# Kernel optimization log

Measured on AMD Instinct MI355X. Metric: run time of the kernel, lower is better.

The kernel has to match this reference:

```python
import jax, jax.numpy as jnp
import numpy as np

B, S, D, E = 4, 4096, 2048, 64
NOISE_STD = 1.0


def setup_inputs() -> dict:
    key = jax.random.key(0)
    k1, k2, k3, k4 = jax.random.split(key, 4)
    x = jax.random.normal(k1, (B, S, D), dtype=jnp.float32)
    lim = float(np.sqrt(6.0 / (D + E)))  # glorot_uniform
    W_gate = jax.random.uniform(k2, (D, E), jnp.float32, -lim, lim)
    # keras inits noise_dense kernel to zeros; use tiny random values so the
    # noise path is numerically exercised (zeros would make it trivially ln(2)).
    W_noise = 0.02 * jax.random.normal(k3, (D, E), dtype=jnp.float32)
    noise = jax.random.normal(k4, (B * S, E), dtype=jnp.float32)
    return {"x": x, "W_gate": W_gate, "W_noise": W_noise, "noise": noise, "top_k": 2}


def reference(x, W_gate, W_noise, noise, top_k):
    b, s, d = x.shape
    e = W_gate.shape[1]
    xf = x.reshape(-1, d)                         # [N, D], N = b*s
    gate_logits = xf @ W_gate                     # [N, E]
    # training-mode noise injection
    noise_logits = xf @ W_noise                   # [N, E]
    nstd = jax.nn.softplus(noise_logits) * (NOISE_STD / (e * e))
    gate_logits = gate_logits + noise * nstd
    # top-k mask + masked softmax
    top_vals, top_idx = jax.lax.top_k(gate_logits, top_k)   # [N, K]
    n = gate_logits.shape[0]
    mask = jnp.zeros_like(gate_logits).at[jnp.arange(n)[:, None], top_idx].set(1.0)
    masked_logits = jnp.where(mask > 0, gate_logits, jnp.float32(-1e9))
    expert_weights = jax.nn.softmax(masked_logits, axis=-1)  # [N, E]
    raw_gate_probs = jax.nn.softmax(gate_logits, axis=-1)    # [N, E]
    expert_weights = expert_weights.reshape(b, s, e)
    expert_indices = top_idx.reshape(b, s, top_k).astype(jnp.int32)
    return expert_weights, expert_indices, gate_logits, raw_gate_probs
```

## Files before the change

kernel.cpp:

```cpp
#include <hip/hip_runtime.h>
#include <math.h>


typedef _Float16 f16;
typedef f16  f16x4  __attribute__((ext_vector_type(4)));
typedef f16  f16x8  __attribute__((ext_vector_type(8)));
typedef float f32x16 __attribute__((ext_vector_type(16)));

constexpr int NROWS = 16384;
constexpr int DDIM  = 2048;
constexpr int NE    = 64;
constexpr int BM    = 32;
constexpr int KI    = 32;
constexpr int NITER = 1024 / KI;
constexpr float NSCALE = 1.0f / 4096.0f;

__device__ __forceinline__ int a_off(int buf, int h, int s, int v) {
    return (((buf * 2 + h) * 2 + s) * 2 + v) * 1024;
}

__device__ __forceinline__ float softplus_f(float x) {
    return fmaxf(x, 0.0f) + log1pf(expf(-fabsf(x)));
}

__device__ __forceinline__ void tile_bar() {
    asm volatile("s_waitcnt lgkmcnt(0)" ::: "memory");
    __builtin_amdgcn_sched_barrier(0);
    __builtin_amdgcn_s_barrier();
    __builtin_amdgcn_sched_barrier(0);
}

__global__ __launch_bounds__(256) void wprep_kernel(
    const float* __restrict__ Wg, const float* __restrict__ Wn,
    f16* __restrict__ ws)
{
    int t = blockIdx.x * 256 + threadIdx.x;
    int S = t >> 8;
    int f = (t >> 6) & 3;
    int l = t & 63;
    int k0  = S * 16 + (l >> 5) * 8;
    int col = f * 32 + (l & 31);
    const float* src = (col < NE) ? (Wg + col) : (Wn + col - NE);
    f16x8 hp, lp;
    #pragma unroll
    for (int j = 0; j < 8; ++j) {
        float w  = src[(size_t)(k0 + j) * NE];
        f16 h    = (f16)w;
        float hf = (float)h;
        hp[j] = h;
        lp[j] = (f16)((w - hf) * 64.0f);
    }
    size_t base = (size_t)(S * 4 + f) * 1024;
    *(f16x8*)(ws + base + l * 8)       = hp;
    *(f16x8*)(ws + base + 512 + l * 8) = lp;
}

__global__ __launch_bounds__(512, 4) void gemm_gating(
    const float* __restrict__ x, const f16* __restrict__ wfrag,
    const float* __restrict__ noise,
    float* __restrict__ out_w, float* __restrict__ out_idx,
    float* __restrict__ out_logits, float* __restrict__ out_probs)
{
    __shared__ __align__(16) char smem[49152];
    const int tid = threadIdx.x;
    const int l   = tid & 63;
    const int w   = tid >> 6;
    const int h   = w >> 2;
    const int f   = w & 3;
    const int row0 = blockIdx.x * BM;

    f32x16 acc1, acc2;
    #pragma unroll
    for (int r = 0; r < 16; ++r) { acc1[r] = 0.0f; acc2[r] = 0.0f; }

    const int h_s = w >> 2, s_s = (w >> 1) & 1, j4 = w & 1;
    const float* aSrc = x + (size_t)(row0 + (l & 31)) * DDIM
                          + h_s * 1024 + s_s * 16 + (l >> 5) * 8 + j4 * 4;
    auto loadA = [&](int t) -> float4 {
        return *(const float4*)(aSrc + (size_t)t * KI);
    };
    auto cvtWrite = [&](float4 xv, int tt) {
        int buf = tt & 3;
        float xs[4] = {xv.x, xv.y, xv.z, xv.w};
        f16x4 hi, lo;
        #pragma unroll
        for (int j = 0; j < 4; ++j) {
            f16 hh   = (f16)xs[j];
            float hf = (float)hh;
            hi[j] = hh;
            lo[j] = (f16)((xs[j] - hf) * 64.0f);
        }
        *(f16x4*)(smem + a_off(buf, h_s, s_s, 0) + l * 16 + j4 * 8) = hi;
        *(f16x4*)(smem + a_off(buf, h_s, s_s, 1) + l * 16 + j4 * 8) = lo;
    };

    const f16* bBase = wfrag + (size_t)f * 1024 + l * 8;
    f16x8 bh0c, bl0c, bh1c, bl1c, bh0n, bl0n, bh1n, bl1n;
    auto loadB = [&](int t, f16x8& H0, f16x8& L0, f16x8& H1, f16x8& L1) {
        const f16* p = bBase + (size_t)(h * 64 + t * 2) * 4096;
        H0 = *(const f16x8*)p;
        L0 = *(const f16x8*)(p + 512);
        H1 = *(const f16x8*)(p + 4096);
        L1 = *(const f16x8*)(p + 4096 + 512);
    };

    auto compute = [&](int t) {
        int buf = t & 3;
        #pragma unroll
        for (int s = 0; s < 2; ++s) {
            f16x8 Ah = *(const f16x8*)(smem + a_off(buf, h, s, 0) + l * 16);
            f16x8 Al = *(const f16x8*)(smem + a_off(buf, h, s, 1) + l * 16);
            f16x8 Bh = s ? bh1c : bh0c;
            f16x8 Bl = s ? bl1c : bl0c;
            acc1 = __builtin_amdgcn_mfma_f32_32x32x16_f16(Ah, Bh, acc1, 0, 0, 0);
            acc2 = __builtin_amdgcn_mfma_f32_32x32x16_f16(Ah, Bl, acc2, 0, 0, 0);
            acc2 = __builtin_amdgcn_mfma_f32_32x32x16_f16(Al, Bh, acc2, 0, 0, 0);
        }
    };

    float4 r0 = loadA(0);
    float4 r1 = loadA(1);
    loadB(0, bh0c, bl0c, bh1c, bl1c);
    float4 sc = loadA(2);
    float4 sm = loadA(3);
    cvtWrite(r0, 0);
    cvtWrite(r1, 1);

    for (int t = 0; t < NITER; ++t) {
        tile_bar();
        float4 sn = sc;
        if (t + 4 < NITER) sn = loadA(t + 4);
        if (t + 1 < NITER) loadB(t + 1, bh0n, bl0n, bh1n, bl1n);
        if (t + 2 < NITER) cvtWrite(sc, t + 2);
        compute(t);
        sc = sm; sm = sn;
        bh0c = bh0n; bl0c = bl0n; bh1c = bh1n; bl1c = bl1n;
    }
    __syncthreads();

    float* mg  = (float*)(smem + 32768);
    if (h == 1) {
        #pragma unroll
        for (int r = 0; r < 16; ++r) {
            float cv = fmaf(acc2[r], 0.015625f, acc1[r]);
            int row = (r & 3) + 8 * (r >> 2) + 4 * (l >> 5);
            int col = f * 32 + (l & 31);
            mg[row * 128 + col] = cv;
        }
    }
    __syncthreads();

    float* lgf = (float*)smem;
    if (h == 0) {
        #pragma unroll
        for (int r = 0; r < 16; ++r) {
            float cv = fmaf(acc2[r], 0.015625f, acc1[r]);
            int row = (r & 3) + 8 * (r >> 2) + 4 * (l >> 5);
            int col = f * 32 + (l & 31);
            lgf[row * 132 + col] = cv + mg[row * 128 + col];
        }
    }
    __syncthreads();

    {
        const int pr = tid & 31;
        const int c4 = tid >> 5;
        const int n1 = row0 + pr;
        float4 G  = *(const float4*)(lgf + pr * 132 + c4 * 4);
        float4 NL = *(const float4*)(lgf + pr * 132 + 64 + c4 * 4);
        float4 NZ = *(const float4*)(noise + (size_t)n1 * NE + c4 * 4);
        G.x += NZ.x * softplus_f(NL.x) * NSCALE;
        G.y += NZ.y * softplus_f(NL.y) * NSCALE;
        G.z += NZ.z * softplus_f(NL.z) * NSCALE;
        G.w += NZ.w * softplus_f(NL.w) * NSCALE;
        *(float4*)(lgf + pr * 132 + c4 * 4) = G;
        *(float4*)(out_logits + (size_t)n1 * NE + c4 * 4) = G;
    }
    __syncthreads();

    if (w < 4) {
        const int g2   = l >> 3;
        const int c    = l & 7;
        const int row2 = w * 8 + g2;
        const int n2   = row0 + row2;

        float mv[8];
        {
            const float4* mr = (const float4*)(lgf + row2 * 132 + c * 8);
            float4 m0 = mr[0], m1 = mr[1];
            mv[0]=m0.x; mv[1]=m0.y; mv[2]=m0.z; mv[3]=m0.w;
            mv[4]=m1.x; mv[5]=m1.y; mv[6]=m1.z; mv[7]=m1.w;
        }
        float v0 = -INFINITY, v1 = -INFINITY;
        int i0 = 0, i1 = 0;
        #pragma unroll
        for (int j = 0; j < 8; ++j) {
            float v = mv[j]; int e = c * 8 + j;
            if (v > v0) { v1 = v0; i1 = i0; v0 = v; i0 = e; }
            else if (v > v1) { v1 = v; i1 = e; }
        }
        #pragma unroll
        for (int m = 1; m <= 4; m <<= 1) {
            float ov0 = __shfl_xor(v0, m), ov1 = __shfl_xor(v1, m);
            int   oi0 = __shfl_xor(i0, m), oi1 = __shfl_xor(i1, m);
            if (ov0 > v0) {
                bool keep = (v0 > ov1);
                v1 = keep ? v0 : ov1; i1 = keep ? i0 : oi1;
                v0 = ov0; i0 = oi0;
            } else if (ov0 > v1) {
                v1 = ov0; i1 = oi0;
            }
        }
        const int srcl = l & 56;
        v0 = __shfl(v0, srcl); i0 = __shfl(i0, srcl);
        v1 = __shfl(v1, srcl); i1 = __shfl(i1, srcl);

        float se = 0.0f;
        #pragma unroll
        for (int j = 0; j < 8; ++j) se += expf(mv[j] - v0);
        se += __shfl_xor(se, 1); se += __shfl_xor(se, 2); se += __shfl_xor(se, 4);
        float inv_se = 1.0f / se;

        float t  = expf(v1 - v0);
        float w0 = 1.0f / (1.0f + t);
        float w1 = t * w0;

        float pr[8], wt[8];
        #pragma unroll
        for (int j = 0; j < 8; ++j) {
            int e = c * 8 + j;
            pr[j] = expf(mv[j] - v0) * inv_se;
            wt[j] = (e == i0) ? w0 : ((e == i1) ? w1 : 0.0f);
        }
        *(float4*)(out_probs + (size_t)n2 * NE + c * 8)     = make_float4(pr[0], pr[1], pr[2], pr[3]);
        *(float4*)(out_probs + (size_t)n2 * NE + c * 8 + 4) = make_float4(pr[4], pr[5], pr[6], pr[7]);
        *(float4*)(out_w + (size_t)n2 * NE + c * 8)         = make_float4(wt[0], wt[1], wt[2], wt[3]);
        *(float4*)(out_w + (size_t)n2 * NE + c * 8 + 4)     = make_float4(wt[4], wt[5], wt[6], wt[7]);
        if (c == 0) {
            *(float2*)(out_idx + (size_t)n2 * 2) = make_float2((float)i0, (float)i1);
        }
    }
}

extern "C" void kernel_launch(void* const* d_in, const int* in_sizes, int n_in,
                              void* d_out, int out_size, void* d_ws, size_t ws_size,
                              hipStream_t stream) {
    (void)in_sizes; (void)n_in; (void)ws_size; (void)out_size;
    const float* x     = (const float*)d_in[0];
    const float* Wg    = (const float*)d_in[1];
    const float* Wn    = (const float*)d_in[2];
    const float* noise = (const float*)d_in[3];
    float* out        = (float*)d_out;
    float* out_w      = out;
    float* out_idx    = out + (size_t)NROWS * NE;
    float* out_logits = out_idx + (size_t)NROWS * 2;
    float* out_probs  = out_logits + (size_t)NROWS * NE;
    f16* wfrag = (f16*)d_ws;

    wprep_kernel<<<128, 256, 0, stream>>>(Wg, Wn, wfrag);
    gemm_gating<<<NROWS / BM, 512, 0, stream>>>(
        x, wfrag, noise, out_w, out_idx, out_logits, out_probs);
}
```

Before: 56.08 us.

## Unroll K-loop by four with static smem buffers and double-buffered B fragments

Restructures the main GEMM loop into a 4-way manually unrolled body with compile-time shared-memory buffer indices and two ping-ponged sets of B-fragment registers. Compute on the current buffer is issued before the next global loads and conversion writes, and the custom lgkmcnt/sched_barrier tile barrier is replaced with plain __syncthreads. The aim is to remove the register rotation copies and dynamic buffer indexing, and to give the scheduler more freedom to overlap loads with MFMA. In exchange it uses more registers and gives up the explicit scheduling barriers, so instruction placement is left to the compiler.

New measurement: 52.52 us. -6.3%, faster.

```diff
diff --git a/kernel.cpp b/kernel.cpp
--- a/kernel.cpp
+++ b/kernel.cpp
@@ -12,7 +12,6 @@
 constexpr int NE    = 64;
 constexpr int BM    = 32;
 constexpr int KI    = 32;
-constexpr int NITER = 1024 / KI;
 constexpr float NSCALE = 1.0f / 4096.0f;
 
 __device__ __forceinline__ int a_off(int buf, int h, int s, int v) {
@@ -21,13 +20,6 @@
 
 __device__ __forceinline__ float softplus_f(float x) {
     return fmaxf(x, 0.0f) + log1pf(expf(-fabsf(x)));
-}
-
-__device__ __forceinline__ void tile_bar() {
-    asm volatile("s_waitcnt lgkmcnt(0)" ::: "memory");
-    __builtin_amdgcn_sched_barrier(0);
-    __builtin_amdgcn_s_barrier();
-    __builtin_amdgcn_sched_barrier(0);
 }
 
 __global__ __launch_bounds__(256) void wprep_kernel(
@@ -79,8 +71,7 @@
     auto loadA = [&](int t) -> float4 {
         return *(const float4*)(aSrc + (size_t)t * KI);
     };
-    auto cvtWrite = [&](float4 xv, int tt) {
-        int buf = tt & 3;
+    auto cvtWrite = [&](float4 xv, int buf) {
         float xs[4] = {xv.x, xv.y, xv.z, xv.w};
         f16x4 hi, lo;
         #pragma unroll
@@ -95,50 +86,65 @@
     };
 
     const f16* bBase = wfrag + (size_t)f * 1024 + l * 8;
-    f16x8 bh0c, bl0c, bh1c, bl1c, bh0n, bl0n, bh1n, bl1n;
-    auto loadB = [&](int t, f16x8& H0, f16x8& L0, f16x8& H1, f16x8& L1) {
-        const f16* p = bBase + (size_t)(h * 64 + t * 2) * 4096;
-        H0 = *(const f16x8*)p;
-        L0 = *(const f16x8*)(p + 512);
-        H1 = *(const f16x8*)(p + 4096);
-        L1 = *(const f16x8*)(p + 4096 + 512);
-    };
-
-    auto compute = [&](int t) {
-        int buf = t & 3;
+#define LOADB(t, H0, L0, H1, L1) do {                                       \
+        const f16* _p = bBase + (size_t)(h * 64 + (t) * 2) * 4096;          \
+        H0 = *(const f16x8*)_p;          L0 = *(const f16x8*)(_p + 512);    \
+        H1 = *(const f16x8*)(_p + 4096); L1 = *(const f16x8*)(_p + 4608);   \
+    } while (0)
+
+    auto compute = [&](int buf, f16x8 Bh0, f16x8 Bl0, f16x8 Bh1, f16x8 Bl1) {
         #pragma unroll
         for (int s = 0; s < 2; ++s) {
             f16x8 Ah = *(const f16x8*)(smem + a_off(buf, h, s, 0) + l * 16);
             f16x8 Al = *(const f16x8*)(smem + a_off(buf, h, s, 1) + l * 16);
-            f16x8 Bh = s ? bh1c : bh0c;
-            f16x8 Bl = s ? bl1c : bl0c;
+            f16x8 Bh = s ? Bh1 : Bh0;
+            f16x8 Bl = s ? Bl1 : Bl0;
             acc1 = __builtin_amdgcn_mfma_f32_32x32x16_f16(Ah, Bh, acc1, 0, 0, 0);
             acc2 = __builtin_amdgcn_mfma_f32_32x32x16_f16(Ah, Bl, acc2, 0, 0, 0);
             acc2 = __builtin_amdgcn_mfma_f32_32x32x16_f16(Al, Bh, acc2, 0, 0, 0);
         }
     };
 
-    float4 r0 = loadA(0);
-    float4 r1 = loadA(1);
-    loadB(0, bh0c, bl0c, bh1c, bl1c);
-    float4 sc = loadA(2);
-    float4 sm = loadA(3);
-    cvtWrite(r0, 0);
-    cvtWrite(r1, 1);
-
-    for (int t = 0; t < NITER; ++t) {
-        tile_bar();
-        float4 sn = sc;
-        if (t + 4 < NITER) sn = loadA(t + 4);
-        if (t + 1 < NITER) loadB(t + 1, bh0n, bl0n, bh1n, bl1n);
-        if (t + 2 < NITER) cvtWrite(sc, t + 2);
-        compute(t);
-        sc = sm; sm = sn;
-        bh0c = bh0n; bl0c = bl0n; bh1c = bh1n; bl1c = bl1n;
-    }
-    __syncthreads();
-
-    float* mg  = (float*)(smem + 32768);
+    float4 a0, a1, a2, a3;
+    f16x8 b0h0, b0l0, b0h1, b0l1;
+    f16x8 b1h0, b1l0, b1h1, b1l1;
+
+    a0 = loadA(0); a1 = loadA(1); a2 = loadA(2); a3 = loadA(3);
+    LOADB(0, b0h0, b0l0, b0h1, b0l1);
+    LOADB(1, b1h0, b1l0, b1h1, b1l1);
+    cvtWrite(a0, 0);
+    cvtWrite(a1, 1);
+    __syncthreads();
+
+    for (int tb = 0; tb < 32; tb += 4) {
+        compute(0, b0h0, b0l0, b0h1, b0l1);
+        if (tb + 4 < 32) a0 = loadA(tb + 4);
+        if (tb + 2 < 32) LOADB(tb + 2, b0h0, b0l0, b0h1, b0l1);
+        cvtWrite(a2, 2);
+        __syncthreads();
+        compute(1, b1h0, b1l0, b1h1, b1l1);
+        if (tb + 5 < 32) a1 = loadA(tb + 5);
+        if (tb + 3 < 32) LOADB(tb + 3, b1h0, b1l0, b1h1, b1l1);
+        cvtWrite(a3, 3);
+        __syncthreads();
+        compute(2, b0h0, b0l0, b0h1, b0l1);
+        if (tb + 6 < 32) a2 = loadA(tb + 6);
+        if (tb + 4 < 32) {
+            LOADB(tb + 4, b0h0, b0l0, b0h1, b0l1);
+            cvtWrite(a0, 0);
+        }
+        __syncthreads();
+        compute(3, b1h0, b1l0, b1h1, b1l1);
+        if (tb + 7 < 32) a3 = loadA(tb + 7);
+        if (tb + 5 < 32) {
+            LOADB(tb + 5, b1h0, b1l0, b1h1, b1l1);
+            cvtWrite(a1, 1);
+        }
+        __syncthreads();
+    }
+#undef LOADB
+
+    float* mg = (float*)(smem + 32768);
     if (h == 1) {
         #pragma unroll
         for (int r = 0; r < 16; ++r) {
```
